# Optimization experiments

Measured on AMD Instinct MI355X. Metric: run time of the kernel, lower is better.

The kernel has to match this reference:

```python
import jax, jax.numpy as jnp
import numpy as np

EPS = 1e-8

def _mlp3(x, w1, b1, w2, b2, w3, b3):
    h = jax.nn.relu(x @ w1.T + b1)
    h = jax.nn.relu(h @ w2.T + b2)
    return h @ w3.T + b3

def _basis_matrix(n_output_features, n_points, dtype):
    # Gaussian RBF basis, identical per batch element: [F, P]
    t = jnp.linspace(0.0, 1.0, n_output_features, dtype=dtype)  # [F]
    if n_points > 1:
        centers = jnp.arange(n_points, dtype=dtype) / (n_points - 1)
    else:
        centers = jnp.full((n_points,), 0.5, dtype=dtype)
    sigma = 1.0 / n_points
    basis = jnp.exp(-((t[:, None] - centers[None, :]) ** 2) / (2.0 * sigma ** 2))
    return basis / (basis.sum(axis=1, keepdims=True) + EPS)

def setup_inputs() -> dict:
    key = jax.random.key(0)
    B, D, P, F = 16384, 128, 10, 1024
    ks = jax.random.split(key, 13)

    def lin(k, fan_in, fan_out):
        bound = 1.0 / np.sqrt(fan_in)
        kw, kb = jax.random.split(k)
        w = jax.random.uniform(kw, (fan_out, fan_in), jnp.float32, -bound, bound)
        b = jax.random.uniform(kb, (fan_out,), jnp.float32, -bound, bound)
        return w, b

    x = jax.random.normal(ks[0], (B, D), jnp.float32)
    cp_w1, cp_b1 = lin(ks[1], D, 128)
    cp_w2, cp_b2 = lin(ks[2], 128, 256)
    cp_w3, cp_b3 = lin(ks[3], 256, P * 2)
    w_w1, w_b1 = lin(ks[4], D, 64)
    w_w2, w_b2 = lin(ks[5], 64, 128)
    w_w3, w_b3 = lin(ks[6], 128, P)
    return {"x": x,
            "cp_w1": cp_w1, "cp_b1": cp_b1, "cp_w2": cp_w2, "cp_b2": cp_b2,
            "cp_w3": cp_w3, "cp_b3": cp_b3,
            "w_w1": w_w1, "w_b1": w_b1, "w_w2": w_w2, "w_b2": w_b2,
            "w_w3": w_w3, "w_b3": w_b3}

def reference(x, cp_w1, cp_b1, cp_w2, cp_b2, cp_w3, cp_b3,
              w_w1, w_b1, w_w2, w_b2, w_w3, w_b3):
    n_points = w_w3.shape[0]
    n_output_features = 1024

    cp_flat = jnp.tanh(_mlp3(x, cp_w1, cp_b1, cp_w2, cp_b2, cp_w3, cp_b3))
    control_points = cp_flat.reshape(-1, n_points, 2)              # [B, P, 2]
    weights = jax.nn.softmax(_mlp3(x, w_w1, w_b1, w_w2, w_b2, w_w3, w_b3), axis=-1)  # [B, P]

    basis = _basis_matrix(n_output_features, n_points, x.dtype)    # [F, P], row-normalized
    cp_mean = control_points.mean(axis=-1)                         # [B, P]

    # out[b,f] = sum_p basis[f,p]*w[b,p]*cp_mean[b,p] / (sum_p basis[f,p]*w[b,p] + eps)
    num = jnp.einsum('fp,bp->bf', basis, weights * cp_mean)
    den = jnp.einsum('fp,bp->bf', basis, weights) + EPS
    return num / den
```

## Files before the change

### kernel.cpp

```cpp
#include <hip/hip_runtime.h>
#include <math.h>

#define EPS 1e-8f

typedef __attribute__((ext_vector_type(8))) short bf16x8;
typedef __attribute__((ext_vector_type(4))) float f32x4;

#define OFF_F1    0
#define OFF_FV1   16384
#define OFF_F2    24576
#define OFF_FV2   57344
#define OFF_F3    65536
#define OFF_FV3   73728
#define OFF_BASIS 75776

__device__ __forceinline__ unsigned short f2bf(float f){
  unsigned u = __float_as_uint(f);
  return (unsigned short)((u + 0x7fffu + ((u >> 16) & 1u)) >> 16);
}
__device__ __forceinline__ float bf2f(unsigned short h){
  return __uint_as_float(((unsigned)h) << 16);
}
__device__ __forceinline__ int fslot(int s, int kt){
  return s ^ kt ^ (((s >> 4) & 1) << 2);
}

__global__ __launch_bounds__(256) void prep_kernel(
    const float* __restrict__ cw1, const float* __restrict__ cw2, const float* __restrict__ cw3,
    const float* __restrict__ ww1, const float* __restrict__ ww2, const float* __restrict__ ww3,
    float* __restrict__ ws)
{
  int id = blockIdx.x * 256 + threadIdx.x;
  unsigned short* wsU = (unsigned short*)ws;
  if (id < 9472) {
    int t = id >> 6, s = id & 63;
    const float* W; int K, N, tloc, dstF, ktbits;
    if (t < 32)       { W = cw1; K = 128; N = 128; tloc = t;       dstF = OFF_F1;  ktbits = 2; }
    else if (t < 48)  { W = ww1; K = 128; N = 64;  tloc = t - 32;  dstF = OFF_FV1; ktbits = 2; }
    else if (t < 112) { W = cw2; K = 128; N = 256; tloc = t - 48;  dstF = OFF_F2;  ktbits = 2; }
    else if (t < 128) { W = ww2; K = 64;  N = 128; tloc = t - 112; dstF = OFF_FV2; ktbits = 1; }
    else if (t < 144) { W = cw3; K = 256; N = 20;  tloc = t - 128; dstF = OFF_F3;  ktbits = 3; }
    else              { W = ww3; K = 128; N = 10;  tloc = t - 144; dstF = OFF_FV3; ktbits = 2; }
    int kt = tloc & ((1 << ktbits) - 1);
    int nt = tloc >> ktbits;
    int row = nt * 16 + (s & 15);
    int kb  = kt * 32 + 8 * (s >> 4);
    bf16x8 hv, lv;
    #pragma unroll
    for (int j = 0; j < 8; ++j) {
      float v = (row < N) ? W[row * K + kb + j] : 0.f;
      unsigned short h = f2bf(v);
      hv[j] = (short)h;
      lv[j] = (short)f2bf(v - bf2f(h));
    }
    unsigned short* dst = wsU + dstF * 2 + tloc * 1024 + s * 8;
    *(bf16x8*)dst = hv;
    *(bf16x8*)(dst + 512) = lv;
    return;
  }
  id -= 9472;
  if (id < 1024) {
    int f = id;
    float tt = (float)f * (1.0f / 1023.0f);
    float v[10]; float s = 0.f;
    #pragma unroll
    for (int p = 0; p < 10; ++p) {
      float d = tt - (float)p * (1.0f / 9.0f);
      float e = expf(-d * d * 50.0f);
      v[p] = e; s += e;
    }
    float inv = 1.0f / (s + EPS);
    #pragma unroll
    for (int p = 0; p < 10; ++p) ws[OFF_BASIS + f*10 + p] = v[p] * inv;
  }
}

#define MFMA __builtin_amdgcn_mfma_f32_16x16x32_bf16

__global__ __launch_bounds__(512, 4) void fused_kernel(
    const float* __restrict__ x,
    const float* __restrict__ cb1, const float* __restrict__ cb2, const float* __restrict__ cb3,
    const float* __restrict__ wb1, const float* __restrict__ wb2, const float* __restrict__ wb3,
    const float* __restrict__ ws, float* __restrict__ out)
{
  __shared__ unsigned short H2A[16384];
  __shared__ unsigned short H1A[8192];
  __shared__ unsigned short HV1A[4096];
  __shared__ unsigned short HV2A[8192];
  __shared__ float vbuf[320];
  __shared__ float cpbuf[640];

  const int tid = threadIdx.x;
  const int l   = tid & 63;
  const int w   = tid >> 6;
  const int g   = l >> 4;
  const int c16 = l & 15;
  const int b0  = blockIdx.x * 32;
  unsigned short* XA = H2A;
  const unsigned short* wsU = (const unsigned short*)ws;

  {
    int r = tid >> 4, k8 = tid & 15;
    const float4* xg = (const float4*)(x + (size_t)(b0 + r) * 128 + k8 * 8);
    float4 v0 = xg[0], v1 = xg[1];
    float xv[8] = {v0.x, v0.y, v0.z, v0.w, v1.x, v1.y, v1.z, v1.w};
    bf16x8 hv, lv;
    #pragma unroll
    for (int j = 0; j < 8; ++j) {
      unsigned short h = f2bf(xv[j]);
      hv[j] = (short)h;
      lv[j] = (short)f2bf(xv[j] - bf2f(h));
    }
    int kt = k8 >> 2;
    int tile = (r >> 4) * 4 + kt;
    int s = (r & 15) + 16 * (k8 & 3);
    unsigned short* dst = XA + tile * 1024 + fslot(s, kt) * 8;
    *(bf16x8*)dst = hv;
    *(bf16x8*)(dst + 512) = lv;
  }

  const int mt  = w >> 2;
  const int ntv = w & 3;
  const int nt0 = (w & 3) * 2, nt1 = nt0 + 1;
  const unsigned short* BV  = wsU + OFF_FV1*2 + (ntv*4)*1024 + l*8;
  const unsigned short* BL0 = wsU + OFF_F1*2  + (nt0*4)*1024 + l*8;
  const unsigned short* BL1 = wsU + OFF_F1*2  + (nt1*4)*1024 + l*8;
  bf16x8 nvh = *(const bf16x8*)BV;        bf16x8 nvl = *(const bf16x8*)(BV + 512);
  bf16x8 n0h = *(const bf16x8*)BL0;       bf16x8 n0l = *(const bf16x8*)(BL0 + 512);
  bf16x8 n1h = *(const bf16x8*)BL1;       bf16x8 n1l = *(const bf16x8*)(BL1 + 512);

  __syncthreads();

  {
    float bv  = wb1[ntv*16 + c16];
    float bl0 = cb1[nt0*16 + c16], bl1 = cb1[nt1*16 + c16];
    f32x4 aVA = {bv, bv, bv, bv},     aVB = {0.f, 0.f, 0.f, 0.f};
    f32x4 aL0A = {bl0, bl0, bl0, bl0}, aL0B = {0.f, 0.f, 0.f, 0.f};
    f32x4 aL1A = {bl1, bl1, bl1, bl1}, aL1B = {0.f, 0.f, 0.f, 0.f};
    #pragma unroll
    for (int kt = 0; kt < 4; ++kt) {
      bf16x8 vh = nvh, vl = nvl, b0h_ = n0h, b0l_ = n0l, b1h_ = n1h, b1l_ = n1l;
      if (kt < 3) {
        nvh = *(const bf16x8*)(BV  + (kt+1)*1024); nvl = *(const bf16x8*)(BV  + (kt+1)*1024 + 512);
        n0h = *(const bf16x8*)(BL0 + (kt+1)*1024); n0l = *(const bf16x8*)(BL0 + (kt+1)*1024 + 512);
        n1h = *(const bf16x8*)(BL1 + (kt+1)*1024); n1l = *(const bf16x8*)(BL1 + (kt+1)*1024 + 512);
      }
      const unsigned short* ap = XA + (mt*4 + kt) * 1024 + fslot(l, kt) * 8;
      bf16x8 ah = *(const bf16x8*)ap;
      bf16x8 al = *(const bf16x8*)(ap + 512);
      aVA = MFMA(ah, vh, aVA, 0,0,0);   aVB = MFMA(ah, vl, aVB, 0,0,0);   aVB = MFMA(al, vh, aVB, 0,0,0);
      aL0A = MFMA(ah, b0h_, aL0A, 0,0,0); aL0B = MFMA(ah, b0l_, aL0B, 0,0,0); aL0B = MFMA(al, b0h_, aL0B, 0,0,0);
      aL1A = MFMA(ah, b1h_, aL1A, 0,0,0); aL1B = MFMA(ah, b1l_, aL1B, 0,0,0); aL1B = MFMA(al, b1h_, aL1B, 0,0,0);
    }
    {
      int kt2 = ntv >> 1;
      int sb = 16 * ((2*ntv + (c16 >> 3)) & 3);
      unsigned short* tb = HV1A + (mt*2 + kt2) * 1024;
      #pragma unroll
      for (int i = 0; i < 4; ++i) {
        float v = fmaxf(aVA[i] + aVB[i], 0.f);
        int idx = fslot(4*g + i + sb, kt2) * 8 + (c16 & 7);
        unsigned short h = f2bf(v);
        tb[idx] = h; tb[512 + idx] = f2bf(v - bf2f(h));
      }
    }
    #pragma unroll
    for (int t2 = 0; t2 < 2; ++t2) {
      int nt = nt0 + t2;
      int kt2 = nt >> 1;
      int sb = 16 * ((2*nt + (c16 >> 3)) & 3);
      unsigned short* tb = H1A + (mt*4 + kt2) * 1024;
      #pragma unroll
      for (int i = 0; i < 4; ++i) {
        float v = t2 ? fmaxf(aL1A[i] + aL1B[i], 0.f) : fmaxf(aL0A[i] + aL0B[i], 0.f);
        int idx = fslot(4*g + i + sb, kt2) * 8 + (c16 & 7);
        unsigned short h = f2bf(v);
        tb[idx] = h; tb[512 + idx] = f2bf(v - bf2f(h));
      }
    }
  }

  const int v0t = (w & 3) * 2, v1t = v0t + 1;
  const unsigned short* C0 = wsU + OFF_FV2*2 + (v0t*2)*1024 + l*8;
  const unsigned short* C1 = wsU + OFF_FV2*2 + (v1t*2)*1024 + l*8;
  bf16x8 c0h0 = *(const bf16x8*)C0;          bf16x8 c0l0 = *(const bf16x8*)(C0 + 512);
  bf16x8 c0h1 = *(const bf16x8*)(C0 + 1024); bf16x8 c0l1 = *(const bf16x8*)(C0 + 1536);
  bf16x8 c1h0 = *(const bf16x8*)C1;          bf16x8 c1l0 = *(const bf16x8*)(C1 + 512);
  bf16x8 c1h1 = *(const bf16x8*)(C1 + 1024); bf16x8 c1l1 = *(const bf16x8*)(C1 + 1536);

  __syncthreads();

  {
    float bb0 = wb2[v0t*16 + c16], bb1 = wb2[v1t*16 + c16];
    f32x4 a0A = {bb0, bb0, bb0, bb0}, a0B = {0.f, 0.f, 0.f, 0.f};
    f32x4 a1A = {bb1, bb1, bb1, bb1}, a1B = {0.f, 0.f, 0.f, 0.f};
    {
      const unsigned short* ap = HV1A + (mt*2 + 0) * 1024 + fslot(l, 0) * 8;
      bf16x8 ah = *(const bf16x8*)ap, al = *(const bf16x8*)(ap + 512);
      a0A = MFMA(ah, c0h0, a0A, 0,0,0); a0B = MFMA(ah, c0l0, a0B, 0,0,0); a0B = MFMA(al, c0h0, a0B, 0,0,0);
      a1A = MFMA(ah, c1h0, a1A, 0,0,0); a1B = MFMA(ah, c1l0, a1B, 0,0,0); a1B = MFMA(al, c1h0, a1B, 0,0,0);
    }
    {
      const unsigned short* ap = HV1A + (mt*2 + 1) * 1024 + fslot(l, 1) * 8;
      bf16x8 ah = *(const bf16x8*)ap, al = *(const bf16x8*)(ap + 512);
      a0A = MFMA(ah, c0h1, a0A, 0,0,0); a0B = MFMA(ah, c0l1, a0B, 0,0,0); a0B = MFMA(al, c0h1, a0B, 0,0,0);
      a1A = MFMA(ah, c1h1, a1A, 0,0,0); a1B = MFMA(ah, c1l1, a1B, 0,0,0); a1B = MFMA(al, c1h1, a1B, 0,0,0);
    }
    #pragma unroll
    for (int t2 = 0; t2 < 2; ++t2) {
      int nt = v0t + t2;
      int kt2 = nt >> 1;
      int sb = 16 * ((2*nt + (c16 >> 3)) & 3);
      unsigned short* tb = HV2A + (mt*4 + kt2) * 1024;
      #pragma unroll
      for (int i = 0; i < 4; ++i) {
        float v = t2 ? fmaxf(a1A[i] + a1B[i], 0.f) : fmaxf(a0A[i] + a0B[i], 0.f);
        int idx = fslot(4*g + i + sb, kt2) * 8 + (c16 & 7);
        unsigned short h = f2bf(v);
        tb[idx] = h; tb[512 + idx] = f2bf(v - bf2f(h));
      }
    }
  }

  #pragma unroll
  for (int pp = 0; pp < 2; ++pp) {
    const int m0 = (w & 3) * 4 + pp * 2, m1 = m0 + 1;
    const unsigned short* D0 = wsU + OFF_F2*2 + (m0*4)*1024 + l*8;
    const unsigned short* D1 = wsU + OFF_F2*2 + (m1*4)*1024 + l*8;
    bf16x8 nd0h = *(const bf16x8*)D0, nd0l = *(const bf16x8*)(D0 + 512);
    bf16x8 nd1h = *(const bf16x8*)D1, nd1l = *(const bf16x8*)(D1 + 512);
    float bb0 = cb2[m0*16 + c16], bb1 = cb2[m1*16 + c16];
    f32x4 a0A = {bb0, bb0, bb0, bb0}, a0B = {0.f, 0.f, 0.f, 0.f};
    f32x4 a1A = {bb1, bb1, bb1, bb1}, a1B = {0.f, 0.f, 0.f, 0.f};
    #pragma unroll
    for (int kt = 0; kt < 4; ++kt) {
      bf16x8 d0h = nd0h, d0l = nd0l, d1h = nd1h, d1l = nd1l;
      if (kt < 3) {
        nd0h = *(const bf16x8*)(D0 + (kt+1)*1024); nd0l = *(const bf16x8*)(D0 + (kt+1)*1024 + 512);
        nd1h = *(const bf16x8*)(D1 + (kt+1)*1024); nd1l = *(const bf16x8*)(D1 + (kt+1)*1024 + 512);
      }
      const unsigned short* ap = H1A + (mt*4 + kt) * 1024 + fslot(l, kt) * 8;
      bf16x8 ah = *(const bf16x8*)ap, al = *(const bf16x8*)(ap + 512);
      a0A = MFMA(ah, d0h, a0A, 0,0,0); a0B = MFMA(ah, d0l, a0B, 0,0,0); a0B = MFMA(al, d0h, a0B, 0,0,0);
      a1A = MFMA(ah, d1h, a1A, 0,0,0); a1B = MFMA(ah, d1l, a1B, 0,0,0); a1B = MFMA(al, d1h, a1B, 0,0,0);
    }
    #pragma unroll
    for (int t2 = 0; t2 < 2; ++t2) {
      int nt = m0 + t2;
      int kt2 = nt >> 1;
      int sb = 16 * ((2*nt + (c16 >> 3)) & 3);
      unsigned short* tb = H2A + (mt*8 + kt2) * 1024;
      #pragma unroll
      for (int i = 0; i < 4; ++i) {
        float v = t2 ? fmaxf(a1A[i] + a1B[i], 0.f) : fmaxf(a0A[i] + a0B[i], 0.f);
        int idx = fslot(4*g + i + sb, kt2) * 8 + (c16 & 7);
        unsigned short h = f2bf(v);
        tb[idx] = h; tb[512 + idx] = f2bf(v - bf2f(h));
      }
    }
  }
  __syncthreads();

  if (w < 4) {
    const int lmt = w >> 1, lnt = w & 1;
    const unsigned short* F3 = wsU + OFF_F3*2 + (lnt*8)*1024 + l*8;
    f32x4 aA = {0.f, 0.f, 0.f, 0.f}, aB = {0.f, 0.f, 0.f, 0.f};
    bf16x8 nbh = *(const bf16x8*)F3, nbl = *(const bf16x8*)(F3 + 512);
    #pragma unroll
    for (int kt = 0; kt < 8; ++kt) {
      bf16x8 bh = nbh, bl = nbl;
      if (kt < 7) {
        nbh = *(const bf16x8*)(F3 + (kt+1)*1024); nbl = *(const bf16x8*)(F3 + (kt+1)*1024 + 512);
      }
      const unsigned short* ap = H2A + (lmt*8 + kt) * 1024 + fslot(l, kt) * 8;
      bf16x8 ah = *(const bf16x8*)ap, al = *(const bf16x8*)(ap + 512);
      aA = MFMA(ah, bh, aA, 0,0,0); aB = MFMA(ah, bl, aB, 0,0,0); aB = MFMA(al, bh, aB, 0,0,0);
    }
    #pragma unroll
    for (int i = 0; i < 4; ++i) {
      int r = lmt*16 + 4*g + i, c = lnt*16 + c16;
      if (c < 20) cpbuf[r*20 + c] = aA[i] + aB[i];
    }
  } else if (w < 6) {
    const int vmt = w - 4;
    const unsigned short* FV = wsU + OFF_FV3*2 + l*8;
    f32x4 aA = {0.f, 0.f, 0.f, 0.f}, aB = {0.f, 0.f, 0.f, 0.f};
    #pragma unroll
    for (int kt = 0; kt < 4; ++kt) {
      bf16x8 bh = *(const bf16x8*)(FV + kt*1024), bl = *(const bf16x8*)(FV + kt*1024 + 512);
      const unsigned short* ap = HV2A + (vmt*4 + kt) * 1024 + fslot(l, kt) * 8;
      bf16x8 ah = *(const bf16x8*)ap, al = *(const bf16x8*)(ap + 512);
      aA = MFMA(ah, bh, aA, 0,0,0); aB = MFMA(ah, bl, aB, 0,0,0); aB = MFMA(al, bh, aB, 0,0,0);
    }
    #pragma unroll
    for (int i = 0; i < 4; ++i) {
      int r = vmt*16 + 4*g + i;
      if (c16 < 10) vbuf[r*10 + c16] = aA[i] + aB[i];
    }
  }
  __syncthreads();

  if (tid < 32) {
    float lg[10]; float m = -1e30f;
    #pragma unroll
    for (int j = 0; j < 10; ++j) { lg[j] = vbuf[tid*10 + j] + wb3[j]; m = fmaxf(m, lg[j]); }
    float s = 0.f;
    #pragma unroll
    for (int j = 0; j < 10; ++j) { float e = expf(lg[j] - m); lg[j] = e; s += e; }
    float inv = __builtin_amdgcn_rcpf(s);
    #pragma unroll
    for (int j = 0; j < 10; ++j) vbuf[tid*10 + j] = lg[j] * inv;
    #pragma unroll
    for (int p = 0; p < 10; ++p) {
      float s0 = cpbuf[tid*20 + 2*p]     + cb3[2*p];
      float s1 = cpbuf[tid*20 + 2*p + 1] + cb3[2*p + 1];
      float cm = 0.5f * (tanhf(s0) + tanhf(s1));
      cpbuf[tid*20 + p] = vbuf[tid*10 + p] * cm;
    }
  }
  __syncthreads();

  {
    const float* BAS = ws + OFF_BASIS;
    const int f0 = tid * 2;
    float bas[20];
    {
      const float4* bp = (const float4*)(BAS + f0 * 10);
      #pragma unroll
      for (int i = 0; i < 5; ++i) {
        float4 v = bp[i];
        bas[4*i+0] = v.x; bas[4*i+1] = v.y; bas[4*i+2] = v.z; bas[4*i+3] = v.w;
      }
    }
    for (int rr = 0; rr < 32; ++rr) {
      float wv[10], wm[10];
      #pragma unroll
      for (int p = 0; p < 10; p += 2) {
        float2 a = *(const float2*)(vbuf + rr*10 + p);
        wv[p] = a.x; wv[p+1] = a.y;
        float2 b = *(const float2*)(cpbuf + rr*20 + p);
        wm[p] = b.x; wm[p+1] = b.y;
      }
      float n0 = 0.f, d0 = EPS, n1 = 0.f, d1 = EPS;
      #pragma unroll
      for (int p = 0; p < 10; ++p) {
        n0 = fmaf(bas[p],      wm[p], n0);
        d0 = fmaf(bas[p],      wv[p], d0);
        n1 = fmaf(bas[10 + p], wm[p], n1);
        d1 = fmaf(bas[10 + p], wv[p], d1);
      }
      float2 o;
      o.x = n0 * __builtin_amdgcn_rcpf(d0);
      o.y = n1 * __builtin_amdgcn_rcpf(d1);
      *(float2*)(out + (size_t)(b0 + rr) * 1024 + f0) = o;
    }
  }
}

extern "C" void kernel_launch(void* const* d_in, const int* in_sizes, int n_in,
                              void* d_out, int out_size, void* d_ws, size_t ws_size,
                              hipStream_t stream)
{
  const float* x   = (const float*)d_in[0];
  const float* cw1 = (const float*)d_in[1];
  const float* cb1 = (const float*)d_in[2];
  const float* cw2 = (const float*)d_in[3];
  const float* cb2 = (const float*)d_in[4];
  const float* cw3 = (const float*)d_in[5];
  const float* cb3 = (const float*)d_in[6];
  const float* ww1 = (const float*)d_in[7];
  const float* wb1 = (const float*)d_in[8];
  const float* ww2 = (const float*)d_in[9];
  const float* wb2 = (const float*)d_in[10];
  const float* ww3 = (const float*)d_in[11];
  const float* wb3 = (const float*)d_in[12];
  float* ws  = (float*)d_ws;
  float* out = (float*)d_out;

  prep_kernel<<<41, 256, 0, stream>>>(cw1, cw2, cw3, ww1, ww2, ww3, ws);
  fused_kernel<<<512, 512, 0, stream>>>(x, cb1, cb2, cb3, wb1, wb2, wb3, ws, out);
}
```

Baseline: 39.21 us.

## Compute basis-weighted epilogue with split-bf16 MFMA instead of scalar FMAs

The final num/den contraction over the 10 control points moves from per-thread scalar FMA loops onto 16x16x32 bf16 MFMA instructions. Basis and per-row weights are split into hi/lo bf16 pairs to keep near-fp32 accuracy. The prep kernel now writes the basis in an MFMA fragment layout and launches more blocks. The epilogue is output-store bound (64MB written), so the compute savings may be hidden, and the hi/lo split adds some precision risk in the division.

```diff
diff --git a/kernel.cpp b/kernel.cpp
--- a/kernel.cpp
+++ b/kernel.cpp
@@ -12,7 +12,7 @@
 #define OFF_FV2   57344
 #define OFF_F3    65536
 #define OFF_FV3   73728
-#define OFF_BASIS 75776
+#define OFF_BASF  75776
 
 __device__ __forceinline__ unsigned short f2bf(float f){
   unsigned u = __float_as_uint(f);
@@ -59,19 +59,31 @@
     return;
   }
   id -= 9472;
-  if (id < 1024) {
-    int f = id;
+  if (id < 4096) {
+    int ft = id >> 6, s = id & 63;
+    int f = ft * 16 + (s & 15);
+    int k0 = 8 * (s >> 4);
     float tt = (float)f * (1.0f / 1023.0f);
-    float v[10]; float s = 0.f;
+    float v[10]; float sum = 0.f;
     #pragma unroll
     for (int p = 0; p < 10; ++p) {
       float d = tt - (float)p * (1.0f / 9.0f);
       float e = expf(-d * d * 50.0f);
-      v[p] = e; s += e;
-    }
-    float inv = 1.0f / (s + EPS);
-    #pragma unroll
-    for (int p = 0; p < 10; ++p) ws[OFF_BASIS + f*10 + p] = v[p] * inv;
+      v[p] = e; sum += e;
+    }
+    float inv = 1.0f / (sum + EPS);
+    bf16x8 hv, lv;
+    #pragma unroll
+    for (int j = 0; j < 8; ++j) {
+      int k = k0 + j;
+      float val = (k < 10) ? v[k] * inv : 0.f;
+      unsigned short h = f2bf(val);
+      hv[j] = (short)h;
+      lv[j] = (short)f2bf(val - bf2f(h));
+    }
+    unsigned short* dst = wsU + OFF_BASF * 2 + ft * 1024 + s * 8;
+    *(bf16x8*)dst = hv;
+    *(bf16x8*)(dst + 512) = lv;
   }
 }
 
@@ -320,39 +332,69 @@
   }
   __syncthreads();
 
+  unsigned short* CB = H1A;
+  if (tid < 256) {
+    int tile = tid >> 6, s = tid & 63;
+    int src = tile >> 1, bt = tile & 1;
+    int b = bt * 16 + (s & 15);
+    int k0 = 8 * (s >> 4);
+    bf16x8 hv, lv;
+    #pragma unroll
+    for (int j = 0; j < 8; ++j) {
+      int k = k0 + j;
+      float v = 0.f;
+      if (k < 10) v = src ? vbuf[b*10 + k] : cpbuf[b*20 + k];
+      unsigned short h = f2bf(v);
+      hv[j] = (short)h;
+      lv[j] = (short)f2bf(v - bf2f(h));
+    }
+    unsigned short* dst = CB + tile * 1024 + s * 8;
+    *(bf16x8*)dst = hv;
+    *(bf16x8*)(dst + 512) = lv;
+  }
+  __syncthreads();
+
   {
-    const float* BAS = ws + OFF_BASIS;
-    const int f0 = tid * 2;
-    float bas[20];
-    {
-      const float4* bp = (const float4*)(BAS + f0 * 10);
-      #pragma unroll
-      for (int i = 0; i < 5; ++i) {
-        float4 v = bp[i];
-        bas[4*i+0] = v.x; bas[4*i+1] = v.y; bas[4*i+2] = v.z; bas[4*i+3] = v.w;
-      }
-    }
-    for (int rr = 0; rr < 32; ++rr) {
-      float wv[10], wm[10];
-      #pragma unroll
-      for (int p = 0; p < 10; p += 2) {
-        float2 a = *(const float2*)(vbuf + rr*10 + p);
-        wv[p] = a.x; wv[p+1] = a.y;
-        float2 b = *(const float2*)(cpbuf + rr*20 + p);
-        wm[p] = b.x; wm[p+1] = b.y;
-      }
-      float n0 = 0.f, d0 = EPS, n1 = 0.f, d1 = EPS;
-      #pragma unroll
-      for (int p = 0; p < 10; ++p) {
-        n0 = fmaf(bas[p],      wm[p], n0);
-        d0 = fmaf(bas[p],      wv[p], d0);
-        n1 = fmaf(bas[10 + p], wm[p], n1);
-        d1 = fmaf(bas[10 + p], wv[p], d1);
-      }
-      float2 o;
-      o.x = n0 * __builtin_amdgcn_rcpf(d0);
-      o.y = n1 * __builtin_amdgcn_rcpf(d1);
-      *(float2*)(out + (size_t)(b0 + rr) * 1024 + f0) = o;
+    bf16x8 wm0h = *(const bf16x8*)(CB + 0*1024 + l*8);
+    bf16x8 wm0l = *(const bf16x8*)(CB + 0*1024 + 512 + l*8);
+    bf16x8 wm1h = *(const bf16x8*)(CB + 1*1024 + l*8);
+    bf16x8 wm1l = *(const bf16x8*)(CB + 1*1024 + 512 + l*8);
+    bf16x8 w0h  = *(const bf16x8*)(CB + 2*1024 + l*8);
+    bf16x8 w0l  = *(const bf16x8*)(CB + 2*1024 + 512 + l*8);
+    bf16x8 w1h  = *(const bf16x8*)(CB + 3*1024 + l*8);
+    bf16x8 w1l  = *(const bf16x8*)(CB + 3*1024 + 512 + l*8);
+    const unsigned short* AP = wsU + OFF_BASF*2 + (w*8)*1024 + l*8;
+    bf16x8 nah = *(const bf16x8*)AP;
+    bf16x8 nal = *(const bf16x8*)(AP + 512);
+    const size_t orow0 = (size_t)(b0 + c16) * 1024 + 4*g;
+    #pragma unroll
+    for (int t = 0; t < 8; ++t) {
+      bf16x8 ah = nah, al = nal;
+      if (t < 7) {
+        nah = *(const bf16x8*)(AP + (t+1)*1024);
+        nal = *(const bf16x8*)(AP + (t+1)*1024 + 512);
+      }
+      const f32x4 z = {0.f, 0.f, 0.f, 0.f};
+      f32x4 n0A = MFMA(ah, wm0h, z, 0,0,0);
+      f32x4 n0B = MFMA(ah, wm0l, z, 0,0,0);  n0B = MFMA(al, wm0h, n0B, 0,0,0);
+      f32x4 d0A = MFMA(ah, w0h,  z, 0,0,0);
+      f32x4 d0B = MFMA(ah, w0l,  z, 0,0,0);  d0B = MFMA(al, w0h,  d0B, 0,0,0);
+      f32x4 n1A = MFMA(ah, wm1h, z, 0,0,0);
+      f32x4 n1B = MFMA(ah, wm1l, z, 0,0,0);  n1B = MFMA(al, wm1h, n1B, 0,0,0);
+      f32x4 d1A = MFMA(ah, w1h,  z, 0,0,0);
+      f32x4 d1B = MFMA(ah, w1l,  z, 0,0,0);  d1B = MFMA(al, w1h,  d1B, 0,0,0);
+      float4 o0, o1;
+      o0.x = (n0A[0]+n0B[0]) * __builtin_amdgcn_rcpf(d0A[0]+d0B[0]+EPS);
+      o0.y = (n0A[1]+n0B[1]) * __builtin_amdgcn_rcpf(d0A[1]+d0B[1]+EPS);
+      o0.z = (n0A[2]+n0B[2]) * __builtin_amdgcn_rcpf(d0A[2]+d0B[2]+EPS);
+      o0.w = (n0A[3]+n0B[3]) * __builtin_amdgcn_rcpf(d0A[3]+d0B[3]+EPS);
+      o1.x = (n1A[0]+n1B[0]) * __builtin_amdgcn_rcpf(d1A[0]+d1B[0]+EPS);
+      o1.y = (n1A[1]+n1B[1]) * __builtin_amdgcn_rcpf(d1A[1]+d1B[1]+EPS);
+      o1.z = (n1A[2]+n1B[2]) * __builtin_amdgcn_rcpf(d1A[2]+d1B[2]+EPS);
+      o1.w = (n1A[3]+n1B[3]) * __builtin_amdgcn_rcpf(d1A[3]+d1B[3]+EPS);
+      int fcol = (w*8 + t) * 16;
+      *(float4*)(out + orow0 + fcol)               = o0;
+      *(float4*)(out + orow0 + 16*1024 + fcol)     = o1;
     }
   }
 }
@@ -377,6 +419,6 @@
   float* ws  = (float*)d_ws;
   float* out = (float*)d_out;
 
-  prep_kernel<<<41, 256, 0, stream>>>(cw1, cw2, cw3, ww1, ww2, ww3, ws);
+  prep_kernel<<<53, 256, 0, stream>>>(cw1, cw2, cw3, ww1, ww2, ww3, ws);
   fused_kernel<<<512, 512, 0, stream>>>(x, cb1, cb2, cb3, wb1, wb2, wb3, ws, out);
 }
```

After: 42.62 us. 1.09x slower.
